# Kernel optimization log

Hardware: AMD Instinct MI355X
Metric: run time of the kernel (lower is better)

## Reference

```python
import jax, jax.numpy as jnp
import numpy as np

N_NODES = 100000
N_EDGES = 1600000
IN_DIM, HID_DIM, OUT_DIM = 32, 16, 8


def setup_inputs() -> dict:
    key = jax.random.key(0)
    ks = jax.random.split(key, 10)
    x = jax.random.normal(ks[0], (N_NODES, IN_DIM), dtype=jnp.float32)
    edge_index = jax.random.randint(ks[1], (2, N_EDGES), 0, N_NODES, dtype=jnp.int32)
    s1 = 1.0 / np.sqrt(IN_DIM)
    s2 = 1.0 / np.sqrt(HID_DIM)
    s3 = 1.0 / np.sqrt(OUT_DIM)
    return {
        "x": x,
        "edge_index": edge_index,
        # SAGEConv layer 1: lin_l (neighbor, with bias) and lin_r (root)
        "Wl1": jax.random.uniform(ks[2], (HID_DIM, IN_DIM), jnp.float32, -s1, s1),
        "bl1": jnp.zeros((HID_DIM,), jnp.float32),
        "Wr1": jax.random.uniform(ks[3], (HID_DIM, IN_DIM), jnp.float32, -s1, s1),
        # SAGEConv layer 2
        "Wl2": jax.random.uniform(ks[4], (OUT_DIM, HID_DIM), jnp.float32, -s2, s2),
        "bl2": jnp.zeros((OUT_DIM,), jnp.float32),
        "Wr2": jax.random.uniform(ks[5], (OUT_DIM, HID_DIM), jnp.float32, -s2, s2),
        # final Linear head
        "Wfc": jax.random.uniform(ks[6], (1, OUT_DIM), jnp.float32, -s3, s3),
        "bfc": jax.random.uniform(ks[7], (1,), jnp.float32, -s3, s3),
    }


def _sage_conv(x, src, dst, Wl, bl, Wr):
    # mean-aggregate neighbor messages x[src] at destination nodes
    msg_sum = jax.ops.segment_sum(x[src], dst, num_segments=N_NODES)  # [N, d]
    deg = jax.ops.segment_sum(jnp.ones((src.shape[0],), x.dtype), dst, num_segments=N_NODES)
    mean = msg_sum / jnp.maximum(deg, 1.0)[:, None]
    # out = lin_l(mean_neighbors) + lin_r(x_root)
    return mean @ Wl.T + bl + x @ Wr.T


def reference(x, edge_index, Wl1, bl1, Wr1, Wl2, bl2, Wr2, Wfc, bfc):
    src, dst = edge_index[0], edge_index[1]
    h = _sage_conv(x, src, dst, Wl1, bl1, Wr1)
    h = jax.nn.relu(h)
    h = _sage_conv(h, src, dst, Wl2, bl2, Wr2)
    return h @ Wfc.T + bfc  # [N, 1]
```

## Files before the change

kernel.cpp:

```cpp
#include <hip/hip_runtime.h>

#define NN 100000
#define NE 1600000
#define IN_DIM 32
#define HID_DIM 16
#define OUT_DIM 8

#define NPB 128
#define NBK ((NN + NPB - 1) / NPB)
#define CAP 3200
#define EPB 4096
#define EPT (EPB / 256)
#define NT_BUCKET ((NE + EPB - 1) / EPB)
#define NT_PRE1 ((NN + 255) / 256)
#define GRID1 (NT_BUCKET + NT_PRE1)
#define BF_STRIDE 16
#define SCAN_CHUNKS ((NBK + 255) / 256)

__global__ __launch_bounds__(256) void k_phase1(
    const float* __restrict__ x, const int* __restrict__ src, const int* __restrict__ dst,
    const float* __restrict__ Wl1, const float* __restrict__ bl1, const float* __restrict__ Wr1,
    const float* __restrict__ Wl2, const float* __restrict__ bl2, const float* __restrict__ Wr2,
    const float* __restrict__ Wfc, const float* __restrict__ bfc,
    int* __restrict__ bucketfill, unsigned int* __restrict__ bucket,
    float* __restrict__ z, float* __restrict__ rb, float* __restrict__ uvc)
{
    __shared__ int lcnt[NBK];
    __shared__ int lpos[NBK];
    __shared__ int lbase[NBK];
    __shared__ int lfill[NBK];
    __shared__ int sscan[256];
    __shared__ unsigned int ssorted[EPB];
    __shared__ unsigned short sbin[EPB];
    int tid = threadIdx.x;

    if (blockIdx.x < NT_BUCKET) {
        int e0 = blockIdx.x * EPB;
        int e1 = min(e0 + EPB, NE);
        int total = e1 - e0;

        for (int i = tid; i < NBK; i += 256) lcnt[i] = 0;
        __syncthreads();

        int myd[EPT];
#pragma unroll
        for (int k = 0; k < EPT; k++) {
            int e = e0 + k * 256 + tid;
            myd[k] = (e < e1) ? dst[e] : -1;
            if (myd[k] >= 0) atomicAdd(&lcnt[myd[k] >> 7], 1);
        }
        __syncthreads();

        int carry = 0;
        for (int ch = 0; ch < SCAN_CHUNKS; ch++) {
            int idx = ch * 256 + tid;
            int v = (idx < NBK) ? lcnt[idx] : 0;
            sscan[tid] = v;
            __syncthreads();
            for (int off = 1; off < 256; off <<= 1) {
                int t2 = (tid >= off) ? sscan[tid - off] : 0;
                __syncthreads();
                sscan[tid] += t2;
                __syncthreads();
            }
            if (idx < NBK) lpos[idx] = carry + sscan[tid] - v;
            carry += sscan[255];
            __syncthreads();
        }

        for (int i = tid; i < NBK; i += 256) {
            lbase[i] = (lcnt[i] > 0) ? atomicAdd(&bucketfill[i * BF_STRIDE], lcnt[i]) : 0;
            lfill[i] = lpos[i];
        }
        __syncthreads();

#pragma unroll
        for (int k = 0; k < EPT; k++) {
            if (myd[k] >= 0) {
                int e = e0 + k * 256 + tid;
                int s = src[e];
                int b = myd[k] >> 7;
                int p = atomicAdd(&lfill[b], 1);
                ssorted[p] = (unsigned)(myd[k] & (NPB - 1)) | ((unsigned)s << 7);
                sbin[p] = (unsigned short)b;
            }
        }
        __syncthreads();

        for (int i = tid; i < total; i += 256) {
            int b = sbin[i];
            bucket[(size_t)b * CAP + lbase[b] + (i - lpos[b])] = ssorted[i];
        }
    } else {
        int chunk = blockIdx.x - NT_BUCKET;
        float* sWl = (float*)ssorted;
        float* sWr = sWl + 512;
        float* sb  = (float*)sbin;
        for (int i = tid; i < HID_DIM * IN_DIM; i += 256) {
            sWl[i] = Wl1[i];
            sWr[i] = Wr1[i];
        }
        if (tid < HID_DIM) sb[tid] = bl1[tid];
        if (chunk == 0) {
            if (tid < HID_DIM) {
                float uu = 0.f, vv = 0.f;
#pragma unroll
                for (int o = 0; o < OUT_DIM; o++) {
                    uu += Wfc[o] * Wl2[o * HID_DIM + tid];
                    vv += Wfc[o] * Wr2[o * HID_DIM + tid];
                }
                uvc[tid] = uu;
                uvc[HID_DIM + tid] = vv;
            }
            if (tid == 0) {
                float c0 = bfc[0];
#pragma unroll
                for (int o = 0; o < OUT_DIM; o++) c0 += Wfc[o] * bl2[o];
                uvc[2 * HID_DIM] = c0;
            }
        }
        __syncthreads();
        int n = chunk * 256 + tid;
        if (n < NN) {
            float xv[IN_DIM];
            const float4* x4 = (const float4*)(x + (size_t)n * IN_DIM);
#pragma unroll
            for (int c = 0; c < 8; c++) {
                float4 b = x4[c];
                xv[c * 4 + 0] = b.x; xv[c * 4 + 1] = b.y;
                xv[c * 4 + 2] = b.z; xv[c * 4 + 3] = b.w;
            }
            float zo[HID_DIM], ro[HID_DIM];
#pragma unroll
            for (int o = 0; o < HID_DIM; o++) {
                float az = 0.f, ar = sb[o];
#pragma unroll
                for (int i = 0; i < IN_DIM; i++) {
                    az += sWl[o * IN_DIM + i] * xv[i];
                    ar += sWr[o * IN_DIM + i] * xv[i];
                }
                zo[o] = az; ro[o] = ar;
            }
            float4* z4 = (float4*)(z + (size_t)n * HID_DIM);
            float4* r4 = (float4*)(rb + (size_t)n * HID_DIM);
#pragma unroll
            for (int c = 0; c < 4; c++) {
                z4[c] = make_float4(zo[c*4], zo[c*4+1], zo[c*4+2], zo[c*4+3]);
                r4[c] = make_float4(ro[c*4], ro[c*4+1], ro[c*4+2], ro[c*4+3]);
            }
        }
    }
}

__global__ __launch_bounds__(256) void k_sort_gather(
    const int* __restrict__ bucketfill, const unsigned int* __restrict__ bucket,
    const float* __restrict__ z, const float* __restrict__ rb, const float* __restrict__ uvc,
    int* __restrict__ deg, float* __restrict__ sv, float* __restrict__ tv)
{
    __shared__ int lcnt[NPB];
    __shared__ int lscan[NPB];
    __shared__ int lfill[NPB];
    __shared__ int ssrc[CAP];

    int b = blockIdx.x;
    int tid = threadIdx.x;
    int cntb = bucketfill[b * BF_STRIDE];
    const unsigned int* bk = bucket + (size_t)b * CAP;

    if (tid < NPB) lcnt[tid] = 0;
    __syncthreads();
    for (int i = tid; i < cntb; i += 256) atomicAdd(&lcnt[bk[i] & (NPB - 1)], 1);
    __syncthreads();
    if (tid < NPB) lscan[tid] = lcnt[tid];
    __syncthreads();
    for (int off = 1; off < NPB; off <<= 1) {
        int tvv = (tid >= off && tid < NPB) ? lscan[tid - off] : 0;
        __syncthreads();
        if (tid < NPB) lscan[tid] += tvv;
        __syncthreads();
    }
    if (tid < NPB) {
        lfill[tid] = lscan[tid] - lcnt[tid];
        int node = b * NPB + tid;
        if (node < NN) deg[node] = lcnt[tid];
    }
    __syncthreads();
    for (int i = tid; i < cntb; i += 256) {
        unsigned v = bk[i];
        int d = v & (NPB - 1);
        int p = atomicAdd(&lfill[d], 1);
        ssrc[p] = (int)(v >> 7);
    }
    __syncthreads();

    int c = tid & 3;
    int nl0 = tid >> 2;
    float4 u4 = ((const float4*)uvc)[c];
    float4 v4 = ((const float4*)uvc)[4 + c];
    const float4* z4p = (const float4*)z;
#pragma unroll
    for (int pass = 0; pass < 2; pass++) {
        int nl = pass * 64 + nl0;
        int n2 = b * NPB + nl;
        if (n2 < NN) {
            int dg = lcnt[nl];
            int st = lscan[nl] - dg;
            float4 acc = {0.f, 0.f, 0.f, 0.f};
            int i = 0;
            for (; i + 4 <= dg; i += 4) {
                int s0 = ssrc[st + i + 0];
                int s1 = ssrc[st + i + 1];
                int s2 = ssrc[st + i + 2];
                int s3 = ssrc[st + i + 3];
                float4 v0 = z4p[s0 * 4 + c];
                float4 v1 = z4p[s1 * 4 + c];
                float4 v2 = z4p[s2 * 4 + c];
                float4 v3 = z4p[s3 * 4 + c];
                acc.x += v0.x + v1.x + v2.x + v3.x;
                acc.y += v0.y + v1.y + v2.y + v3.y;
                acc.z += v0.z + v1.z + v2.z + v3.z;
                acc.w += v0.w + v1.w + v2.w + v3.w;
            }
            for (; i < dg; i++) {
                float4 vz = z4p[ssrc[st + i] * 4 + c];
                acc.x += vz.x; acc.y += vz.y; acc.z += vz.z; acc.w += vz.w;
            }
            float inv = 1.0f / fmaxf((float)dg, 1.0f);
            float4 r = ((const float4*)rb)[n2 * 4 + c];
            float h0 = fmaxf(acc.x * inv + r.x, 0.f);
            float h1 = fmaxf(acc.y * inv + r.y, 0.f);
            float h2 = fmaxf(acc.z * inv + r.z, 0.f);
            float h3 = fmaxf(acc.w * inv + r.w, 0.f);
            float ps = u4.x * h0 + u4.y * h1 + u4.z * h2 + u4.w * h3;
            float pt = v4.x * h0 + v4.y * h1 + v4.z * h2 + v4.w * h3;
            ps += __shfl_xor(ps, 1);
            ps += __shfl_xor(ps, 2);
            pt += __shfl_xor(pt, 1);
            pt += __shfl_xor(pt, 2);
            if (c == 0) { sv[n2] = ps; tv[n2] = pt; }
        }
    }
}

__global__ __launch_bounds__(256) void k_final(
    const int* __restrict__ bucketfill, const unsigned int* __restrict__ bucket,
    const int* __restrict__ deg, const float* __restrict__ sv, const float* __restrict__ tv,
    const float* __restrict__ uvc, float* __restrict__ out)
{
    __shared__ float lsum[NPB];
    int b = blockIdx.x;
    int tid = threadIdx.x;
    int cntb = bucketfill[b * BF_STRIDE];
    const unsigned int* bk = bucket + (size_t)b * CAP;

    if (tid < NPB) lsum[tid] = 0.f;
    __syncthreads();
    for (int i = tid; i < cntb; i += 256) {
        unsigned v = bk[i];
        int d = v & (NPB - 1);
        int s = (int)(v >> 7);
        atomicAdd(&lsum[d], sv[s]);
    }
    __syncthreads();
    if (tid < NPB) {
        int n = b * NPB + tid;
        if (n < NN) {
            float dg = (float)deg[n];
            out[n] = lsum[tid] / fmaxf(dg, 1.0f) + tv[n] + uvc[2 * HID_DIM];
        }
    }
}

extern "C" void kernel_launch(void* const* d_in, const int* in_sizes, int n_in,
                              void* d_out, int out_size, void* d_ws, size_t ws_size,
                              hipStream_t stream) {
    const float* x   = (const float*)d_in[0];
    const int*   ei  = (const int*)d_in[1];
    const float* Wl1 = (const float*)d_in[2];
    const float* bl1 = (const float*)d_in[3];
    const float* Wr1 = (const float*)d_in[4];
    const float* Wl2 = (const float*)d_in[5];
    const float* bl2 = (const float*)d_in[6];
    const float* Wr2 = (const float*)d_in[7];
    const float* Wfc = (const float*)d_in[8];
    const float* bfc = (const float*)d_in[9];
    float* out = (float*)d_out;

    const int* src = ei;
    const int* dst = ei + NE;

    int* bucketfill = (int*)d_ws;
    int* deg        = bucketfill + 12544;
    float* uvc      = (float*)(deg + NN);
    float* sv       = uvc + 40;
    float* tv       = sv + NN;
    unsigned int* bucket = (unsigned int*)(tv + NN);
    float* z        = (float*)(bucket + (size_t)NBK * CAP);
    float* rb       = z + (size_t)NN * HID_DIM;

    hipMemsetAsync(bucketfill, 0, NBK * BF_STRIDE * sizeof(int), stream);

    k_phase1<<<GRID1, 256, 0, stream>>>(x, src, dst, Wl1, bl1, Wr1,
                                        Wl2, bl2, Wr2, Wfc, bfc,
                                        bucketfill, bucket, z, rb, uvc);
    k_sort_gather<<<NBK, 256, 0, stream>>>(bucketfill, bucket, z, rb, uvc, deg, sv, tv);
    k_final<<<NBK, 256, 0, stream>>>(bucketfill, bucket, deg, sv, tv, uvc, out);
}
```

Measured before the change: 159.2 us.

## Replace per-bucket counting sort with shared-memory atomic scatter-add aggregation

The layer-1 aggregation kernel no longer counting-sorts each bucket's edges by destination and then gathers per node. Instead it stages the bucket in LDS and has 16 lanes per edge fetch the source's 16-float z row and atomically add it into a per-node LDS accumulator, counting degrees the same way. This removes the histogram, the scan, the scatter pass and several barriers. In exchange it adds many LDS float atomics, which can contend on high-degree nodes, and uses scalar rather than float4 global loads.

```diff
diff --git a/kernel.cpp b/kernel.cpp
--- a/kernel.cpp
+++ b/kernel.cpp
@@ -152,81 +152,70 @@
     }
 }
 
-__global__ __launch_bounds__(256) void k_sort_gather(
+__global__ __launch_bounds__(256) void k_aggregate(
     const int* __restrict__ bucketfill, const unsigned int* __restrict__ bucket,
     const float* __restrict__ z, const float* __restrict__ rb, const float* __restrict__ uvc,
     int* __restrict__ deg, float* __restrict__ sv, float* __restrict__ tv)
 {
+    __shared__ float lacc[NPB * HID_DIM];
     __shared__ int lcnt[NPB];
-    __shared__ int lscan[NPB];
-    __shared__ int lfill[NPB];
-    __shared__ int ssrc[CAP];
+    __shared__ unsigned int sbk[CAP];
 
     int b = blockIdx.x;
     int tid = threadIdx.x;
     int cntb = bucketfill[b * BF_STRIDE];
     const unsigned int* bk = bucket + (size_t)b * CAP;
 
+    for (int i = tid; i < NPB * HID_DIM; i += 256) lacc[i] = 0.f;
     if (tid < NPB) lcnt[tid] = 0;
+    for (int i = tid; i < cntb; i += 256) sbk[i] = bk[i];
     __syncthreads();
-    for (int i = tid; i < cntb; i += 256) atomicAdd(&lcnt[bk[i] & (NPB - 1)], 1);
+
+    int c = tid & 15;
+    int slot = tid >> 4;
+
+    int e = slot;
+    for (; e + 48 < cntb; e += 64) {
+        unsigned v0 = sbk[e];
+        unsigned v1 = sbk[e + 16];
+        unsigned v2 = sbk[e + 32];
+        unsigned v3 = sbk[e + 48];
+        float f0 = z[(v0 >> 7) * HID_DIM + c];
+        float f1 = z[(v1 >> 7) * HID_DIM + c];
+        float f2 = z[(v2 >> 7) * HID_DIM + c];
+        float f3 = z[(v3 >> 7) * HID_DIM + c];
+        atomicAdd(&lacc[((v0 & (NPB - 1)) << 4) + c], f0);
+        atomicAdd(&lacc[((v1 & (NPB - 1)) << 4) + c], f1);
+        atomicAdd(&lacc[((v2 & (NPB - 1)) << 4) + c], f2);
+        atomicAdd(&lacc[((v3 & (NPB - 1)) << 4) + c], f3);
+        if (c == 0) {
+            atomicAdd(&lcnt[v0 & (NPB - 1)], 1);
+            atomicAdd(&lcnt[v1 & (NPB - 1)], 1);
+            atomicAdd(&lcnt[v2 & (NPB - 1)], 1);
+            atomicAdd(&lcnt[v3 & (NPB - 1)], 1);
+        }
+    }
+    for (; e < cntb; e += 16) {
+        unsigned v = sbk[e];
+        float f = z[(v >> 7) * HID_DIM + c];
+        atomicAdd(&lacc[((v & (NPB - 1)) << 4) + c], f);
+        if (c == 0) atomicAdd(&lcnt[v & (NPB - 1)], 1);
+    }
     __syncthreads();
-    if (tid < NPB) lscan[tid] = lcnt[tid];
-    __syncthreads();
-    for (int off = 1; off < NPB; off <<= 1) {
-        int tvv = (tid >= off && tid < NPB) ? lscan[tid - off] : 0;
-        __syncthreads();
-        if (tid < NPB) lscan[tid] += tvv;
-        __syncthreads();
-    }
-    if (tid < NPB) {
-        lfill[tid] = lscan[tid] - lcnt[tid];
-        int node = b * NPB + tid;
-        if (node < NN) deg[node] = lcnt[tid];
-    }
-    __syncthreads();
-    for (int i = tid; i < cntb; i += 256) {
-        unsigned v = bk[i];
-        int d = v & (NPB - 1);
-        int p = atomicAdd(&lfill[d], 1);
-        ssrc[p] = (int)(v >> 7);
-    }
-    __syncthreads();
-
-    int c = tid & 3;
+
+    int c4 = tid & 3;
     int nl0 = tid >> 2;
-    float4 u4 = ((const float4*)uvc)[c];
-    float4 v4 = ((const float4*)uvc)[4 + c];
-    const float4* z4p = (const float4*)z;
+    float4 u4 = ((const float4*)uvc)[c4];
+    float4 v4 = ((const float4*)uvc)[4 + c4];
 #pragma unroll
     for (int pass = 0; pass < 2; pass++) {
         int nl = pass * 64 + nl0;
         int n2 = b * NPB + nl;
         if (n2 < NN) {
             int dg = lcnt[nl];
-            int st = lscan[nl] - dg;
-            float4 acc = {0.f, 0.f, 0.f, 0.f};
-            int i = 0;
-            for (; i + 4 <= dg; i += 4) {
-                int s0 = ssrc[st + i + 0];
-                int s1 = ssrc[st + i + 1];
-                int s2 = ssrc[st + i + 2];
-                int s3 = ssrc[st + i + 3];
-                float4 v0 = z4p[s0 * 4 + c];
-                float4 v1 = z4p[s1 * 4 + c];
-                float4 v2 = z4p[s2 * 4 + c];
-                float4 v3 = z4p[s3 * 4 + c];
-                acc.x += v0.x + v1.x + v2.x + v3.x;
-                acc.y += v0.y + v1.y + v2.y + v3.y;
-                acc.z += v0.z + v1.z + v2.z + v3.z;
-                acc.w += v0.w + v1.w + v2.w + v3.w;
-            }
-            for (; i < dg; i++) {
-                float4 vz = z4p[ssrc[st + i] * 4 + c];
-                acc.x += vz.x; acc.y += vz.y; acc.z += vz.z; acc.w += vz.w;
-            }
+            float4 acc = ((const float4*)lacc)[nl * 4 + c4];
             float inv = 1.0f / fmaxf((float)dg, 1.0f);
-            float4 r = ((const float4*)rb)[n2 * 4 + c];
+            float4 r = ((const float4*)rb)[n2 * 4 + c4];
             float h0 = fmaxf(acc.x * inv + r.x, 0.f);
             float h1 = fmaxf(acc.y * inv + r.y, 0.f);
             float h2 = fmaxf(acc.z * inv + r.z, 0.f);
@@ -237,7 +226,11 @@
             ps += __shfl_xor(ps, 2);
             pt += __shfl_xor(pt, 1);
             pt += __shfl_xor(pt, 2);
-            if (c == 0) { sv[n2] = ps; tv[n2] = pt; }
+            if (c4 == 0) {
+                sv[n2] = ps;
+                tv[n2] = pt;
+                deg[n2] = dg;
+            }
         }
     }
 }
@@ -303,6 +296,6 @@
     k_phase1<<<GRID1, 256, 0, stream>>>(x, src, dst, Wl1, bl1, Wr1,
                                         Wl2, bl2, Wr2, Wfc, bfc,
                                         bucketfill, bucket, z, rb, uvc);
-    k_sort_gather<<<NBK, 256, 0, stream>>>(bucketfill, bucket, z, rb, uvc, deg, sv, tv);
+    k_aggregate<<<NBK, 256, 0, stream>>>(bucketfill, bucket, z, rb, uvc, deg, sv, tv);
     k_final<<<NBK, 256, 0, stream>>>(bucketfill, bucket, deg, sv, tv, uvc, out);
 }
```

After: 314.9 us. +97.9%, slower.
